# Kernel tuning notes

Hardware: AMD Instinct MI355X
Metric: run time of the kernel (lower is better)

The kernel has to match this reference:

```python
import jax, jax.numpy as jnp
import numpy as np

S, N, IN = 4096, 32, 4
H, IF, SF, OUT = 64, 8, 4, 2
N_PAIRS = N * (N - 1)


def setup_inputs() -> dict:
    key = jax.random.key(0)
    ks = jax.random.split(key, 12)
    f = jax.random.normal
    return {
        "inputs": f(ks[0], (S, N, IN), jnp.float32),
        "L1W": f(ks[1], (H, IN), jnp.float32) * 0.1,
        "L1b": f(ks[2], (H,), jnp.float32) * 0.1,
        "L2W": f(ks[3], (H, H), jnp.float32) * 0.1,
        "L2b": f(ks[4], (H,), jnp.float32) * 0.1,
        "I1W": f(ks[5], (H, H), jnp.float32) * 0.1,
        "I2W": f(ks[6], (IF, H), jnp.float32) * 0.1,
        "I3": f(ks[7], (N_PAIRS, OUT, IF // OUT), jnp.float32) * 0.01,
        "S1W": f(ks[8], (SF, IN), jnp.float32) * 0.1,
        "S1b": f(ks[9], (SF,), jnp.float32) * 0.1,
        "S2W": f(ks[10], (N, OUT, SF // OUT), jnp.float32) * 0.01,
        "S2b": jnp.zeros((N, OUT), jnp.float32),
    }


def reference(inputs, L1W, L1b, L2W, L2b, I1W, I2W, I3, S1W, S1b, S2W, S2b):
    seq_len, n_obj = inputs.shape[:2]
    out_size = S2b.shape[1]

    # shared encoders (torch Linear: x @ W.T + b)
    h = jax.nn.relu(inputs @ L1W.T + L1b)
    h = jax.nn.relu(h @ L2W.T + L2b)          # [S, N, H]
    hs = jax.nn.relu(inputs @ S1W.T + S1b)    # [S, N, SF]

    # all pairwise differences Xi - Xj -> edge MLP (no biases)
    diff = h[:, :, None, :] - h[:, None, :, :]      # [S, N, N, H]
    pair = jnp.tanh(diff @ I1W.T)                   # [S, N, N, H]
    pair = jnp.tanh(pair @ I2W.T)                   # [S, N, N, IF]
    k_int = pair.shape[-1] // out_size
    pair = pair.reshape(seq_len, n_obj, n_obj, out_size, k_int)

    # scatter per-pair weights I3 into dense [N, N, OUT, k] using the
    # row-major Table ordering (i, j != i); diagonal stays zero, which
    # matches the original since diag pairwise features are exactly 0.
    ii, jj = np.nonzero(~np.eye(n_obj, dtype=bool))
    I3d = jnp.zeros((n_obj, n_obj, out_size, k_int), I3.dtype).at[ii, jj].set(I3)

    interaction = jnp.einsum('sijdk,ijdk->sid', pair, I3d)  # [S, N, OUT]

    k_self = hs.shape[-1] // out_size
    hs = hs.reshape(seq_len, n_obj, out_size, k_self)
    self_term = jnp.einsum('sidk,idk->sid', hs, S2W) + S2b  # [S, N, OUT]

    return interaction + self_term
```

## Files before the change

### kernel.cpp

```cpp
#include <hip/hip_runtime.h>
#include <math.h>

#define SEQ   4096
#define NOBJ  32
#define IN_F  4
#define HID   64
#define IFEAT 8
#define NPAIR_HALF 496
#define NTILE 31

#define TWO_LOG2E 2.8853900817779268f
#define GP_CLAMP  10.0f

#if __has_builtin(__builtin_amdgcn_exp2f)
  #define EXP2F(x) __builtin_amdgcn_exp2f(x)
#else
  #define EXP2F(x) exp2f(x)
#endif

typedef _Float16 h2    __attribute__((ext_vector_type(2)));
typedef _Float16 f16x8 __attribute__((ext_vector_type(8)));
typedef short    s16x8 __attribute__((ext_vector_type(8)));
typedef float    f32x4 __attribute__((ext_vector_type(4)));

__device__ __forceinline__ h2 pack2(float a, float b) {
  return __builtin_bit_cast(h2, __builtin_amdgcn_cvt_pkrtz(a, b));
}
__device__ __forceinline__ unsigned pbits(h2 v) { return __builtin_bit_cast(unsigned, v); }

__device__ __forceinline__ f16x8 pack8(float4 a, float4 b) {
  int4 v;
  v.x = (int)pbits(pack2(a.x, a.y));
  v.y = (int)pbits(pack2(a.z, a.w));
  v.z = (int)pbits(pack2(b.x, b.y));
  v.w = (int)pbits(pack2(b.z, b.w));
  return __builtin_bit_cast(f16x8, v);
}

__device__ __forceinline__ f16x8 rcp8nr(f16x8 x) {
  const s16x8 magic = (short)0x7799;
  f16x8 r = __builtin_bit_cast(f16x8, (s16x8)(magic - __builtin_bit_cast(s16x8, x)));
  const f16x8 two = (_Float16)2.0f;
  const f16x8 nx = -x;
#if __has_builtin(__builtin_elementwise_fma)
  r = r * __builtin_elementwise_fma(nx, r, two);
  r = r * __builtin_elementwise_fma(nx, r, two);
#else
  r = r * (nx * r + two);
  r = r * (nx * r + two);
#endif
  return r;
}

__device__ __forceinline__ float dot2h(h2 a, h2 b, float c) {
#if __has_builtin(__builtin_amdgcn_fdot2)
  return __builtin_amdgcn_fdot2(a, b, c, false);
#else
  float r = c;
  r = fmaf((float)a.x, (float)b.x, r);
  r = fmaf((float)a.y, (float)b.y, r);
  return r;
#endif
}

__device__ __forceinline__ float xor8_f32(float v) {
#if __has_builtin(__builtin_amdgcn_mov_dpp)
  return __builtin_bit_cast(float,
      __builtin_amdgcn_mov_dpp(__builtin_bit_cast(int, v), 0x128, 0xF, 0xF, true));
#else
  return __shfl_xor(v, 8, 16);
#endif
}

__device__ __forceinline__ int pair_cum(int i) { return (i * (63 - i)) >> 1; }

__device__ __forceinline__ void pair_decode(int q, int& i, int& j) {
  int ii = (int)((63.0f - sqrtf(3969.0f - 8.0f * (float)q)) * 0.5f);
  if (ii > 0 && pair_cum(ii) > q) --ii;
  if (pair_cum(ii + 1) <= q)     ++ii;
  i = ii;
  j = ii + 1 + (q - pair_cum(ii));
}

__global__ __launch_bounds__(256, 4) void magnet_fused(
    const float* __restrict__ x,
    const float* __restrict__ L1W,
    const float* __restrict__ L1b,
    const float* __restrict__ L2W,
    const float* __restrict__ L2b,
    const float* __restrict__ I1W,
    const float* __restrict__ I2W,
    const float* __restrict__ I3,
    const float* __restrict__ S1W,
    const float* __restrict__ S1b,
    const float* __restrict__ S2W,
    const float* __restrict__ S2b,
    float* __restrict__ out)
{
  __shared__ __align__(16) float smem[8536];
  unsigned*       sEd0 = (unsigned*)(smem + 4960);
  unsigned*       wB   = (unsigned*)(smem + 7264);
  float*          part = smem + 7264;
  float*          sW   = smem + 8032;
  unsigned*       ptab32 = (unsigned*)(smem + 8040);
  float*          swpart = smem + 4960;

  const int t  = threadIdx.x;
  const int s0 = blockIdx.x * 2;

  if (t < 64) {
    const int f = t >> 3, seg = t & 7;
    const float4 a = *(const float4*)(I2W + f * HID + seg * 8);
    const float4 b = *(const float4*)(I2W + f * HID + seg * 8 + 4);
    swpart[t] = ((a.x + a.y) + (a.z + a.w)) + ((b.x + b.y) + (b.z + b.w));
  }
  #pragma unroll
  for (int idx = t; idx < 512; idx += 256) {
    const int n = idx >> 5, k2 = idx & 31;
    wB[idx] = (n < IFEAT)
      ? pbits(pack2(I2W[n * HID + 2 * k2], I2W[n * HID + 2 * k2 + 1])) : 0u;
  }
  #pragma unroll
  for (int q = t; q < NPAIR_HALF; q += 256) {
    int i, j; pair_decode(q, i, j);
    ptab32[q] = ((unsigned)(i * 36) << 16) | (unsigned)(j * 36);
  }

  {
    const int n = t & 31, gI = t >> 5, kb = gI * 8;
    const float4 xv0 = *(const float4*)(x + s0 * 128 + n * 4);
    const float4 xv1 = *(const float4*)(x + s0 * 128 + 128 + n * 4);
    float a[2][8];
    #pragma unroll
    for (int r = 0; r < 8; ++r) {
      const int k = kb + r;
      const float4 w = *(const float4*)(L1W + k * 4);
      const float bias = L1b[k];
      float v0 = bias, v1 = bias;
      v0 = fmaf(xv0.x, w.x, v0); v0 = fmaf(xv0.y, w.y, v0);
      v0 = fmaf(xv0.z, w.z, v0); v0 = fmaf(xv0.w, w.w, v0);
      v1 = fmaf(xv1.x, w.x, v1); v1 = fmaf(xv1.y, w.y, v1);
      v1 = fmaf(xv1.z, w.z, v1); v1 = fmaf(xv1.w, w.w, v1);
      a[0][r] = fmaxf(v0, 0.0f);
      a[1][r] = fmaxf(v1, 0.0f);
    }
    #pragma unroll
    for (int ss = 0; ss < 2; ++ss) {
      unsigned* sAtp = (unsigned*)(smem + ss * 1152);
      int4 pk;
      pk.x = (int)pbits(pack2(a[ss][0], a[ss][1]));
      pk.y = (int)pbits(pack2(a[ss][2], a[ss][3]));
      pk.z = (int)pbits(pack2(a[ss][4], a[ss][5]));
      pk.w = (int)pbits(pack2(a[ss][6], a[ss][7]));
      *(int4*)(sAtp + n * 36 + gI * 4) = pk;
    }
  }
  __syncthreads();

  if (t < IFEAT) {
    float a = 0.0f;
    #pragma unroll
    for (int c = 0; c < 8; ++c) a += swpart[t * 8 + c];
    sW[t] = a;
  }

  const int lane = t & 63;
  const int wv   = t >> 6;
  const int qd   = lane >> 4;
  const int ln   = lane & 15;

  {
    const int m = 16 * wv + ln;
    const float* wr = L2W + m * HID;
    const f16x8 A0 = pack8(*(const float4*)(wr + 8 * qd),
                           *(const float4*)(wr + 8 * qd + 4));
    const f16x8 A1 = pack8(*(const float4*)(wr + 32 + 8 * qd),
                           *(const float4*)(wr + 32 + 8 * qd + 4));
    const float4 bias = *(const float4*)(L2b + 16 * wv + 4 * qd);
    #pragma unroll
    for (int ss = 0; ss < 2; ++ss) {
      const unsigned* sAtp = (const unsigned*)(smem + ss * 1152);
      unsigned* sBtp = (unsigned*)(smem + 2480 + ss * 1152);
      #pragma unroll
      for (int nt = 0; nt < 2; ++nt) {
        const int n = nt * 16 + ln;
        const f16x8 B0 = __builtin_bit_cast(f16x8, *(const int4*)(sAtp + n * 36 + 4 * qd));
        const f16x8 B1 = __builtin_bit_cast(f16x8, *(const int4*)(sAtp + n * 36 + 16 + 4 * qd));
        f32x4 c; c[0] = bias.x; c[1] = bias.y; c[2] = bias.z; c[3] = bias.w;
        c = __builtin_amdgcn_mfma_f32_16x16x32_f16(A0, B0, c, 0, 0, 0);
        c = __builtin_amdgcn_mfma_f32_16x16x32_f16(A1, B1, c, 0, 0, 0);
        sBtp[n * 36 + 8 * wv + 2 * qd]     = pbits(pack2(fmaxf(c[0], 0.f), fmaxf(c[1], 0.f)));
        sBtp[n * 36 + 8 * wv + 2 * qd + 1] = pbits(pack2(fmaxf(c[2], 0.f), fmaxf(c[3], 0.f)));
      }
    }
  }
  __syncthreads();

  {
    const int m = 16 * wv + ln;
    const float* wr = I1W + m * HID;
    float4 w0 = *(const float4*)(wr + 8 * qd);
    float4 w1 = *(const float4*)(wr + 8 * qd + 4);
    float4 w2 = *(const float4*)(wr + 32 + 8 * qd);
    float4 w3 = *(const float4*)(wr + 32 + 8 * qd + 4);
    const float T = TWO_LOG2E;
    w0.x *= T; w0.y *= T; w0.z *= T; w0.w *= T;
    w1.x *= T; w1.y *= T; w1.z *= T; w1.w *= T;
    w2.x *= T; w2.y *= T; w2.z *= T; w2.w *= T;
    w3.x *= T; w3.y *= T; w3.z *= T; w3.w *= T;
    const f16x8 A0 = pack8(w0, w1);
    const f16x8 A1 = pack8(w2, w3);
    #pragma unroll
    for (int ss = 0; ss < 2; ++ss) {
      const unsigned* sBtp = (const unsigned*)(smem + 2480 + ss * 1152);
      unsigned* sEd = sEd0 + ss * 1152;
      #pragma unroll
      for (int nt = 0; nt < 2; ++nt) {
        const int n = nt * 16 + ln;
        const f16x8 B0 = __builtin_bit_cast(f16x8, *(const int4*)(sBtp + n * 36 + 4 * qd));
        const f16x8 B1 = __builtin_bit_cast(f16x8, *(const int4*)(sBtp + n * 36 + 16 + 4 * qd));
        f32x4 c; c[0] = 0.f; c[1] = 0.f; c[2] = 0.f; c[3] = 0.f;
        c = __builtin_amdgcn_mfma_f32_16x16x32_f16(A0, B0, c, 0, 0, 0);
        c = __builtin_amdgcn_mfma_f32_16x16x32_f16(A1, B1, c, 0, 0, 0);
        float e[4];
        #pragma unroll
        for (int r = 0; r < 4; ++r) {
          float gp = fminf(fmaxf(c[r], -GP_CLAMP), GP_CLAMP);
          e[r] = EXP2F(gp);
        }
        sEd[n * 36 + 8 * wv + 2 * qd]     = pbits(pack2(e[0], e[1]));
        sEd[n * 36 + 8 * wv + 2 * qd + 1] = pbits(pack2(e[2], e[3]));
      }
    }
  }
  __syncthreads();

  {
    const f16x8 B0 = __builtin_bit_cast(f16x8, *(const int4*)(wB + ln * 32 + 4 * qd));
    const f16x8 B1 = __builtin_bit_cast(f16x8, *(const int4*)(wB + ln * 32 + 16 + 4 * qd));
    const float WfT = sW[ln & 7] * TWO_LOG2E;
    const float n2T = -2.0f * TWO_LOG2E;
    const bool lo = (ln < IFEAT);
    _Float16* svb = lo ? (_Float16*)smem : (_Float16*)(smem + 2480);
    const int col = ln & 7;

    unsigned pijr[8];
    #pragma unroll
    for (int it = 0; it < 8; ++it) {
      const int tl = wv + it * 4;
      pijr[it] = ptab32[(tl < NTILE ? tl : 0) * 16 + ln];
    }

    #pragma unroll 2
    for (int it = 0; it < 8; ++it) {
      const int tile = wv + it * 4;
      if (tile < NTILE) {
        const unsigned pij = pijr[it];
        const int io = (int)(pij >> 16), jo = (int)(pij & 0xffffu);
        f32x4 c0, c1;
        #pragma unroll
        for (int ss = 0; ss < 2; ++ss) {
          const unsigned* sEd = sEd0 + ss * 1152;
          const f16x8 ei0 = __builtin_bit_cast(f16x8, *(const int4*)(sEd + io + 4 * qd));
          const f16x8 ei1 = __builtin_bit_cast(f16x8, *(const int4*)(sEd + io + 16 + 4 * qd));
          const f16x8 fj0 = __builtin_bit_cast(f16x8, *(const int4*)(sEd + jo + 4 * qd));
          const f16x8 fj1 = __builtin_bit_cast(f16x8, *(const int4*)(sEd + jo + 16 + 4 * qd));
          const f16x8 su0 = ei0 + fj0;
          const f16x8 su1 = ei1 + fj1;
          const f16x8 A0 = fj0 * rcp8nr(su0);
          const f16x8 A1 = fj1 * rcp8nr(su1);
          f32x4 c; c[0] = 0.f; c[1] = 0.f; c[2] = 0.f; c[3] = 0.f;
          c = __builtin_amdgcn_mfma_f32_16x16x32_f16(A0, B0, c, 0, 0, 0);
          c = __builtin_amdgcn_mfma_f32_16x16x32_f16(A1, B1, c, 0, 0, 0);
          if (ss == 0) c0 = c; else c1 = c;
        }
        #pragma unroll
        for (int r = 0; r < 4; ++r) {
          const float c1s = xor8_f32(c1[r]);
          const float m = lo ? c0[r] : c1s;
          const float arg = fmaf(n2T, m, WfT);
          const float e = EXP2F(arg);
          const float rr = __builtin_amdgcn_rcpf(e + 1.0f);
          const float v = fmaf(-2.0f, rr, 1.0f);
          svb[(tile * 16 + 4 * qd + r) * 10 + col] = (_Float16)v;
        }
      }
    }
  }
  __syncthreads();

  {
    const int ss = t >> 7, i = (t >> 2) & 31, d = (t >> 1) & 1, half = t & 1;
    const _Float16* sv = ss ? (const _Float16*)(smem + 2480) : (const _Float16*)smem;
    const int msta = half * 16;
    const int Ci = pair_cum(i);
    float sum = 0.0f;
    #pragma unroll
    for (int it = 0; it < 16; ++it) {
      const int m = msta + it;
      if (m < 31) {
        const bool up = (m >= i);
        const int q = up ? (Ci + m - i) : (pair_cum(m) + i - m - 1);
        const h2* vp = (const h2*)(sv + q * 10 + d * 4);
        const h2 va = vp[0], vb = vp[1];
        const float4 cf = *(const float4*)(I3 + (i * 31 + m) * 8 + d * 4);
        const h2 ca = pack2(cf.x, cf.y);
        const h2 cb = pack2(cf.z, cf.w);
        float dot = dot2h(va, ca, 0.0f);
        dot = dot2h(vb, cb, dot);
        const float sgn = up ? 1.0f : -1.0f;
        sum = fmaf(sgn, dot, sum);
      }
    }
    part[t] = sum;
  }
  __syncthreads();

  if (t < 128) {
    const int ss = t >> 6, i = (t >> 1) & 31, d = t & 1;
    const int pbase = ss * 128 + i * 4 + d * 2;
    float sum = part[pbase] + part[pbase + 1];

    float res = S2b[i * 2 + d] + sum;
    const float4 xv = *(const float4*)(x + (s0 + ss) * 128 + i * 4);
    #pragma unroll
    for (int k = 0; k < 2; ++k) {
      const int f = d * 2 + k;
      float hs = S1b[f];
      hs = fmaf(xv.x, S1W[f * 4 + 0], hs);
      hs = fmaf(xv.y, S1W[f * 4 + 1], hs);
      hs = fmaf(xv.z, S1W[f * 4 + 2], hs);
      hs = fmaf(xv.w, S1W[f * 4 + 3], hs);
      hs = fmaxf(hs, 0.0f);
      res = fmaf(hs, S2W[i * 4 + d * 2 + k], res);
    }
    out[(s0 + ss) * (NOBJ * 2) + i * 2 + d] = res;
  }
}

extern "C" void kernel_launch(void* const* d_in, const int* in_sizes, int n_in,
                              void* d_out, int out_size, void* d_ws, size_t ws_size,
                              hipStream_t stream) {
  const float* x   = (const float*)d_in[0];
  const float* L1W = (const float*)d_in[1];
  const float* L1b = (const float*)d_in[2];
  const float* L2W = (const float*)d_in[3];
  const float* L2b = (const float*)d_in[4];
  const float* I1W = (const float*)d_in[5];
  const float* I2W = (const float*)d_in[6];
  const float* I3  = (const float*)d_in[7];
  const float* S1W = (const float*)d_in[8];
  const float* S1b = (const float*)d_in[9];
  const float* S2W = (const float*)d_in[10];
  const float* S2b = (const float*)d_in[11];
  float* outp = (float*)d_out;

  magnet_fused<<<SEQ / 2, 256, 0, stream>>>(x, L1W, L1b, L2W, L2b, I1W, I2W, I3,
                                            S1W, S1b, S2W, S2b, outp);
}
```

Before: 108.9 us.

## Split the two sequences across wave groups using 512-thread blocks

Blocks grow from 256 to 512 threads, and each group of four waves now handles one of the block's two sequence steps instead of looping over both. This covers the L1/L2/I1 encoders, the pairwise MFMA stage and the final I3 reduction, which now uses four partial sums per output instead of two. In the pair stage, the low and high lanes split the MFMA output rows between them through the xor-8 exchange, so the old cross-sequence select is no longer needed. The goal is to shorten each thread's serial work and raise the number of waves in flight. The cost is higher register pressure under launch_bounds(512,4), and synchronisation barriers now span twice as many waves.

```diff
diff --git a/kernel.cpp b/kernel.cpp
--- a/kernel.cpp
+++ b/kernel.cpp
@@ -82,7 +82,7 @@
   j = ii + 1 + (q - pair_cum(ii));
 }
 
-__global__ __launch_bounds__(256, 4) void magnet_fused(
+__global__ __launch_bounds__(512, 4) void magnet_fused(
     const float* __restrict__ x,
     const float* __restrict__ L1W,
     const float* __restrict__ L1b,
@@ -114,46 +114,36 @@
     const float4 b = *(const float4*)(I2W + f * HID + seg * 8 + 4);
     swpart[t] = ((a.x + a.y) + (a.z + a.w)) + ((b.x + b.y) + (b.z + b.w));
   }
-  #pragma unroll
-  for (int idx = t; idx < 512; idx += 256) {
-    const int n = idx >> 5, k2 = idx & 31;
-    wB[idx] = (n < IFEAT)
+  {
+    const int n = t >> 5, k2 = t & 31;
+    wB[t] = (n < IFEAT)
       ? pbits(pack2(I2W[n * HID + 2 * k2], I2W[n * HID + 2 * k2 + 1])) : 0u;
   }
-  #pragma unroll
-  for (int q = t; q < NPAIR_HALF; q += 256) {
-    int i, j; pair_decode(q, i, j);
-    ptab32[q] = ((unsigned)(i * 36) << 16) | (unsigned)(j * 36);
-  }
-
-  {
-    const int n = t & 31, gI = t >> 5, kb = gI * 8;
-    const float4 xv0 = *(const float4*)(x + s0 * 128 + n * 4);
-    const float4 xv1 = *(const float4*)(x + s0 * 128 + 128 + n * 4);
-    float a[2][8];
+  if (t < NPAIR_HALF) {
+    int i, j; pair_decode(t, i, j);
+    ptab32[t] = ((unsigned)(i * 36) << 16) | (unsigned)(j * 36);
+  }
+
+  {
+    const int n = t & 31, gI = (t >> 5) & 7, ssp = t >> 8, kb = gI * 8;
+    const float4 xv = *(const float4*)(x + s0 * 128 + ssp * 128 + n * 4);
+    float a[8];
     #pragma unroll
     for (int r = 0; r < 8; ++r) {
       const int k = kb + r;
       const float4 w = *(const float4*)(L1W + k * 4);
-      const float bias = L1b[k];
-      float v0 = bias, v1 = bias;
-      v0 = fmaf(xv0.x, w.x, v0); v0 = fmaf(xv0.y, w.y, v0);
-      v0 = fmaf(xv0.z, w.z, v0); v0 = fmaf(xv0.w, w.w, v0);
-      v1 = fmaf(xv1.x, w.x, v1); v1 = fmaf(xv1.y, w.y, v1);
-      v1 = fmaf(xv1.z, w.z, v1); v1 = fmaf(xv1.w, w.w, v1);
-      a[0][r] = fmaxf(v0, 0.0f);
-      a[1][r] = fmaxf(v1, 0.0f);
-    }
-    #pragma unroll
-    for (int ss = 0; ss < 2; ++ss) {
-      unsigned* sAtp = (unsigned*)(smem + ss * 1152);
-      int4 pk;
-      pk.x = (int)pbits(pack2(a[ss][0], a[ss][1]));
-      pk.y = (int)pbits(pack2(a[ss][2], a[ss][3]));
-      pk.z = (int)pbits(pack2(a[ss][4], a[ss][5]));
-      pk.w = (int)pbits(pack2(a[ss][6], a[ss][7]));
-      *(int4*)(sAtp + n * 36 + gI * 4) = pk;
-    }
+      float v = L1b[k];
+      v = fmaf(xv.x, w.x, v); v = fmaf(xv.y, w.y, v);
+      v = fmaf(xv.z, w.z, v); v = fmaf(xv.w, w.w, v);
+      a[r] = fmaxf(v, 0.0f);
+    }
+    unsigned* sAtp = (unsigned*)(smem + ssp * 1152);
+    int4 pk;
+    pk.x = (int)pbits(pack2(a[0], a[1]));
+    pk.y = (int)pbits(pack2(a[2], a[3]));
+    pk.z = (int)pbits(pack2(a[4], a[5]));
+    pk.w = (int)pbits(pack2(a[6], a[7]));
+    *(int4*)(sAtp + n * 36 + gI * 4) = pk;
   }
   __syncthreads();
 
@@ -166,38 +156,37 @@
 
   const int lane = t & 63;
   const int wv   = t >> 6;
+  const int wq   = wv & 3;
+  const int ssw  = wv >> 2;
   const int qd   = lane >> 4;
   const int ln   = lane & 15;
 
   {
-    const int m = 16 * wv + ln;
+    const int m = 16 * wq + ln;
     const float* wr = L2W + m * HID;
     const f16x8 A0 = pack8(*(const float4*)(wr + 8 * qd),
                            *(const float4*)(wr + 8 * qd + 4));
     const f16x8 A1 = pack8(*(const float4*)(wr + 32 + 8 * qd),
                            *(const float4*)(wr + 32 + 8 * qd + 4));
-    const float4 bias = *(const float4*)(L2b + 16 * wv + 4 * qd);
-    #pragma unroll
-    for (int ss = 0; ss < 2; ++ss) {
-      const unsigned* sAtp = (const unsigned*)(smem + ss * 1152);
-      unsigned* sBtp = (unsigned*)(smem + 2480 + ss * 1152);
-      #pragma unroll
-      for (int nt = 0; nt < 2; ++nt) {
-        const int n = nt * 16 + ln;
-        const f16x8 B0 = __builtin_bit_cast(f16x8, *(const int4*)(sAtp + n * 36 + 4 * qd));
-        const f16x8 B1 = __builtin_bit_cast(f16x8, *(const int4*)(sAtp + n * 36 + 16 + 4 * qd));
-        f32x4 c; c[0] = bias.x; c[1] = bias.y; c[2] = bias.z; c[3] = bias.w;
-        c = __builtin_amdgcn_mfma_f32_16x16x32_f16(A0, B0, c, 0, 0, 0);
-        c = __builtin_amdgcn_mfma_f32_16x16x32_f16(A1, B1, c, 0, 0, 0);
-        sBtp[n * 36 + 8 * wv + 2 * qd]     = pbits(pack2(fmaxf(c[0], 0.f), fmaxf(c[1], 0.f)));
-        sBtp[n * 36 + 8 * wv + 2 * qd + 1] = pbits(pack2(fmaxf(c[2], 0.f), fmaxf(c[3], 0.f)));
-      }
-    }
-  }
-  __syncthreads();
-
-  {
-    const int m = 16 * wv + ln;
+    const float4 bias = *(const float4*)(L2b + 16 * wq + 4 * qd);
+    const unsigned* sAtp = (const unsigned*)(smem + ssw * 1152);
+    unsigned* sBtp = (unsigned*)(smem + 2480 + ssw * 1152);
+    #pragma unroll
+    for (int nt = 0; nt < 2; ++nt) {
+      const int n = nt * 16 + ln;
+      const f16x8 B0 = __builtin_bit_cast(f16x8, *(const int4*)(sAtp + n * 36 + 4 * qd));
+      const f16x8 B1 = __builtin_bit_cast(f16x8, *(const int4*)(sAtp + n * 36 + 16 + 4 * qd));
+      f32x4 c; c[0] = bias.x; c[1] = bias.y; c[2] = bias.z; c[3] = bias.w;
+      c = __builtin_amdgcn_mfma_f32_16x16x32_f16(A0, B0, c, 0, 0, 0);
+      c = __builtin_amdgcn_mfma_f32_16x16x32_f16(A1, B1, c, 0, 0, 0);
+      sBtp[n * 36 + 8 * wq + 2 * qd]     = pbits(pack2(fmaxf(c[0], 0.f), fmaxf(c[1], 0.f)));
+      sBtp[n * 36 + 8 * wq + 2 * qd + 1] = pbits(pack2(fmaxf(c[2], 0.f), fmaxf(c[3], 0.f)));
+    }
+  }
+  __syncthreads();
+
+  {
+    const int m = 16 * wq + ln;
     const float* wr = I1W + m * HID;
     float4 w0 = *(const float4*)(wr + 8 * qd);
     float4 w1 = *(const float4*)(wr + 8 * qd + 4);
@@ -210,27 +199,24 @@
     w3.x *= T; w3.y *= T; w3.z *= T; w3.w *= T;
     const f16x8 A0 = pack8(w0, w1);
     const f16x8 A1 = pack8(w2, w3);
-    #pragma unroll
-    for (int ss = 0; ss < 2; ++ss) {
-      const unsigned* sBtp = (const unsigned*)(smem + 2480 + ss * 1152);
-      unsigned* sEd = sEd0 + ss * 1152;
+    const unsigned* sBtp = (const unsigned*)(smem + 2480 + ssw * 1152);
+    unsigned* sEd = sEd0 + ssw * 1152;
+    #pragma unroll
+    for (int nt = 0; nt < 2; ++nt) {
+      const int n = nt * 16 + ln;
+      const f16x8 B0 = __builtin_bit_cast(f16x8, *(const int4*)(sBtp + n * 36 + 4 * qd));
+      const f16x8 B1 = __builtin_bit_cast(f16x8, *(const int4*)(sBtp + n * 36 + 16 + 4 * qd));
+      f32x4 c; c[0] = 0.f; c[1] = 0.f; c[2] = 0.f; c[3] = 0.f;
+      c = __builtin_amdgcn_mfma_f32_16x16x32_f16(A0, B0, c, 0, 0, 0);
+      c = __builtin_amdgcn_mfma_f32_16x16x32_f16(A1, B1, c, 0, 0, 0);
+      float e[4];
       #pragma unroll
-      for (int nt = 0; nt < 2; ++nt) {
-        const int n = nt * 16 + ln;
-        const f16x8 B0 = __builtin_bit_cast(f16x8, *(const int4*)(sBtp + n * 36 + 4 * qd));
-        const f16x8 B1 = __builtin_bit_cast(f16x8, *(const int4*)(sBtp + n * 36 + 16 + 4 * qd));
-        f32x4 c; c[0] = 0.f; c[1] = 0.f; c[2] = 0.f; c[3] = 0.f;
-        c = __builtin_amdgcn_mfma_f32_16x16x32_f16(A0, B0, c, 0, 0, 0);
-        c = __builtin_amdgcn_mfma_f32_16x16x32_f16(A1, B1, c, 0, 0, 0);
-        float e[4];
-        #pragma unroll
-        for (int r = 0; r < 4; ++r) {
-          float gp = fminf(fmaxf(c[r], -GP_CLAMP), GP_CLAMP);
-          e[r] = EXP2F(gp);
-        }
-        sEd[n * 36 + 8 * wv + 2 * qd]     = pbits(pack2(e[0], e[1]));
-        sEd[n * 36 + 8 * wv + 2 * qd + 1] = pbits(pack2(e[2], e[3]));
+      for (int r = 0; r < 4; ++r) {
+        float gp = fminf(fmaxf(c[r], -GP_CLAMP), GP_CLAMP);
+        e[r] = EXP2F(gp);
       }
+      sEd[n * 36 + 8 * wq + 2 * qd]     = pbits(pack2(e[0], e[1]));
+      sEd[n * 36 + 8 * wq + 2 * qd + 1] = pbits(pack2(e[2], e[3]));
     }
   }
   __syncthreads();
@@ -241,48 +227,44 @@
     const float WfT = sW[ln & 7] * TWO_LOG2E;
     const float n2T = -2.0f * TWO_LOG2E;
     const bool lo = (ln < IFEAT);
-    _Float16* svb = lo ? (_Float16*)smem : (_Float16*)(smem + 2480);
+    const unsigned* sEd = sEd0 + ssw * 1152;
+    _Float16* svb = ssw ? (_Float16*)(smem + 2480) : (_Float16*)smem;
     const int col = ln & 7;
+    const int rofs = lo ? 0 : 1;
 
     unsigned pijr[8];
     #pragma unroll
     for (int it = 0; it < 8; ++it) {
-      const int tl = wv + it * 4;
+      const int tl = wq + it * 4;
       pijr[it] = ptab32[(tl < NTILE ? tl : 0) * 16 + ln];
     }
 
     #pragma unroll 2
     for (int it = 0; it < 8; ++it) {
-      const int tile = wv + it * 4;
+      const int tile = wq + it * 4;
       if (tile < NTILE) {
         const unsigned pij = pijr[it];
         const int io = (int)(pij >> 16), jo = (int)(pij & 0xffffu);
-        f32x4 c0, c1;
+        const f16x8 ei0 = __builtin_bit_cast(f16x8, *(const int4*)(sEd + io + 4 * qd));
+        const f16x8 ei1 = __builtin_bit_cast(f16x8, *(const int4*)(sEd + io + 16 + 4 * qd));
+        const f16x8 fj0 = __builtin_bit_cast(f16x8, *(const int4*)(sEd + jo + 4 * qd));
+        const f16x8 fj1 = __builtin_bit_cast(f16x8, *(const int4*)(sEd + jo + 16 + 4 * qd));
+        const f16x8 su0 = ei0 + fj0;
+        const f16x8 su1 = ei1 + fj1;
+        const f16x8 A0 = fj0 * rcp8nr(su0);
+        const f16x8 A1 = fj1 * rcp8nr(su1);
+        f32x4 c; c[0] = 0.f; c[1] = 0.f; c[2] = 0.f; c[3] = 0.f;
+        c = __builtin_amdgcn_mfma_f32_16x16x32_f16(A0, B0, c, 0, 0, 0);
+        c = __builtin_amdgcn_mfma_f32_16x16x32_f16(A1, B1, c, 0, 0, 0);
         #pragma unroll
-        for (int ss = 0; ss < 2; ++ss) {
-          const unsigned* sEd = sEd0 + ss * 1152;
-          const f16x8 ei0 = __builtin_bit_cast(f16x8, *(const int4*)(sEd + io + 4 * qd));
-          const f16x8 ei1 = __builtin_bit_cast(f16x8, *(const int4*)(sEd + io + 16 + 4 * qd));
-          const f16x8 fj0 = __builtin_bit_cast(f16x8, *(const int4*)(sEd + jo + 4 * qd));
-          const f16x8 fj1 = __builtin_bit_cast(f16x8, *(const int4*)(sEd + jo + 16 + 4 * qd));
-          const f16x8 su0 = ei0 + fj0;
-          const f16x8 su1 = ei1 + fj1;
-          const f16x8 A0 = fj0 * rcp8nr(su0);
-          const f16x8 A1 = fj1 * rcp8nr(su1);
-          f32x4 c; c[0] = 0.f; c[1] = 0.f; c[2] = 0.f; c[3] = 0.f;
-          c = __builtin_amdgcn_mfma_f32_16x16x32_f16(A0, B0, c, 0, 0, 0);
-          c = __builtin_amdgcn_mfma_f32_16x16x32_f16(A1, B1, c, 0, 0, 0);
-          if (ss == 0) c0 = c; else c1 = c;
-        }
-        #pragma unroll
-        for (int r = 0; r < 4; ++r) {
-          const float c1s = xor8_f32(c1[r]);
-          const float m = lo ? c0[r] : c1s;
+        for (int rb = 0; rb < 4; rb += 2) {
+          const float cns = xor8_f32(c[rb + 1]);
+          const float m = lo ? c[rb] : cns;
           const float arg = fmaf(n2T, m, WfT);
           const float e = EXP2F(arg);
           const float rr = __builtin_amdgcn_rcpf(e + 1.0f);
           const float v = fmaf(-2.0f, rr, 1.0f);
-          svb[(tile * 16 + 4 * qd + r) * 10 + col] = (_Float16)v;
+          svb[(tile * 16 + 4 * qd + rb + rofs) * 10 + col] = (_Float16)v;
         }
       }
     }
@@ -290,13 +272,13 @@
   __syncthreads();
 
   {
-    const int ss = t >> 7, i = (t >> 2) & 31, d = (t >> 1) & 1, half = t & 1;
-    const _Float16* sv = ss ? (const _Float16*)(smem + 2480) : (const _Float16*)smem;
-    const int msta = half * 16;
+    const int ssp = t >> 8, i = (t >> 3) & 31, d = (t >> 2) & 1, mq = t & 3;
+    const _Float16* sv = ssp ? (const _Float16*)(smem + 2480) : (const _Float16*)smem;
+    const int msta = mq * 8;
     const int Ci = pair_cum(i);
     float sum = 0.0f;
     #pragma unroll
-    for (int it = 0; it < 16; ++it) {
+    for (int it = 0; it < 8; ++it) {
       const int m = msta + it;
       if (m < 31) {
         const bool up = (m >= i);
@@ -317,12 +299,12 @@
   __syncthreads();
 
   if (t < 128) {
-    const int ss = t >> 6, i = (t >> 1) & 31, d = t & 1;
-    const int pbase = ss * 128 + i * 4 + d * 2;
-    float sum = part[pbase] + part[pbase + 1];
+    const int ssp = t >> 6, i = (t >> 1) & 31, d = t & 1;
+    const int pbase = ssp * 256 + i * 8 + d * 4;
+    float sum = (part[pbase] + part[pbase + 1]) + (part[pbase + 2] + part[pbase + 3]);
 
     float res = S2b[i * 2 + d] + sum;
-    const float4 xv = *(const float4*)(x + (s0 + ss) * 128 + i * 4);
+    const float4 xv = *(const float4*)(x + (s0 + ssp) * 128 + i * 4);
     #pragma unroll
     for (int k = 0; k < 2; ++k) {
       const int f = d * 2 + k;
@@ -334,7 +316,7 @@
       hs = fmaxf(hs, 0.0f);
       res = fmaf(hs, S2W[i * 4 + d * 2 + k], res);
     }
-    out[(s0 + ss) * (NOBJ * 2) + i * 2 + d] = res;
+    out[(s0 + ssp) * (NOBJ * 2) + i * 2 + d] = res;
   }
 }
 
@@ -355,6 +337,6 @@
   const float* S2b = (const float*)d_in[11];
   float* outp = (float*)d_out;
 
-  magnet_fused<<<SEQ / 2, 256, 0, stream>>>(x, L1W, L1b, L2W, L2b, I1W, I2W, I3,
+  magnet_fused<<<SEQ / 2, 512, 0, stream>>>(x, L1W, L1b, L2W, L2b, I1W, I2W, I3,
                                             S1W, S1b, S2W, S2b, outp);
 }
```

After: 116.3 us. 1.07x slower.

## Process four sequence steps per block and drop the partial-sum reduction stage

Applied to the files above, without the earlier changes.

Each block now handles four sequence positions instead of two, which halves the grid and reuses the per-block weight setup (I2W packing, pair table, L2W/I1W fragments) across more work. Shared memory grows to about 62KB, which may reduce blocks per CU below the launch_bounds target. The final interaction reduction now has one thread per (s,i,d) loop over all 31 partners, removing a separate partial-sum pass and one barrier at the cost of longer serial loops. The pair-tile loop also drops the register-prefetched pair table in favour of direct loads.

```diff
diff --git a/kernel.cpp b/kernel.cpp
--- a/kernel.cpp
+++ b/kernel.cpp
@@ -97,16 +97,15 @@
     const float* __restrict__ S2b,
     float* __restrict__ out)
 {
-  __shared__ __align__(16) float smem[8536];
-  unsigned*       sEd0 = (unsigned*)(smem + 4960);
-  unsigned*       wB   = (unsigned*)(smem + 7264);
-  float*          part = smem + 7264;
-  float*          sW   = smem + 8032;
-  unsigned*       ptab32 = (unsigned*)(smem + 8040);
-  float*          swpart = smem + 4960;
+  __shared__ __align__(16) float smem[15544];
+  unsigned*       sEd0 = (unsigned*)(smem + 9920);
+  unsigned*       wB   = (unsigned*)(smem + 14528);
+  float*          sW   = smem + 15040;
+  unsigned*       ptab32 = (unsigned*)(smem + 15048);
+  float*          swpart = smem + 9920;
 
   const int t  = threadIdx.x;
-  const int s0 = blockIdx.x * 2;
+  const int s0 = blockIdx.x * 4;
 
   if (t < 64) {
     const int f = t >> 3, seg = t & 7;
@@ -128,24 +127,26 @@
 
   {
     const int n = t & 31, gI = t >> 5, kb = gI * 8;
-    const float4 xv0 = *(const float4*)(x + s0 * 128 + n * 4);
-    const float4 xv1 = *(const float4*)(x + s0 * 128 + 128 + n * 4);
-    float a[2][8];
+    float4 xv[4];
+    #pragma unroll
+    for (int ss = 0; ss < 4; ++ss)
+      xv[ss] = *(const float4*)(x + (s0 + ss) * 128 + n * 4);
+    float a[4][8];
     #pragma unroll
     for (int r = 0; r < 8; ++r) {
       const int k = kb + r;
       const float4 w = *(const float4*)(L1W + k * 4);
       const float bias = L1b[k];
-      float v0 = bias, v1 = bias;
-      v0 = fmaf(xv0.x, w.x, v0); v0 = fmaf(xv0.y, w.y, v0);
-      v0 = fmaf(xv0.z, w.z, v0); v0 = fmaf(xv0.w, w.w, v0);
-      v1 = fmaf(xv1.x, w.x, v1); v1 = fmaf(xv1.y, w.y, v1);
-      v1 = fmaf(xv1.z, w.z, v1); v1 = fmaf(xv1.w, w.w, v1);
-      a[0][r] = fmaxf(v0, 0.0f);
-      a[1][r] = fmaxf(v1, 0.0f);
-    }
-    #pragma unroll
-    for (int ss = 0; ss < 2; ++ss) {
+      #pragma unroll
+      for (int ss = 0; ss < 4; ++ss) {
+        float v = bias;
+        v = fmaf(xv[ss].x, w.x, v); v = fmaf(xv[ss].y, w.y, v);
+        v = fmaf(xv[ss].z, w.z, v); v = fmaf(xv[ss].w, w.w, v);
+        a[ss][r] = fmaxf(v, 0.0f);
+      }
+    }
+    #pragma unroll
+    for (int ss = 0; ss < 4; ++ss) {
       unsigned* sAtp = (unsigned*)(smem + ss * 1152);
       int4 pk;
       pk.x = (int)pbits(pack2(a[ss][0], a[ss][1]));
@@ -178,9 +179,9 @@
                            *(const float4*)(wr + 32 + 8 * qd + 4));
     const float4 bias = *(const float4*)(L2b + 16 * wv + 4 * qd);
     #pragma unroll
-    for (int ss = 0; ss < 2; ++ss) {
+    for (int ss = 0; ss < 4; ++ss) {
       const unsigned* sAtp = (const unsigned*)(smem + ss * 1152);
-      unsigned* sBtp = (unsigned*)(smem + 2480 + ss * 1152);
+      unsigned* sBtp = (unsigned*)(smem + 4608 + ss * 1152);
       #pragma unroll
       for (int nt = 0; nt < 2; ++nt) {
         const int n = nt * 16 + ln;
@@ -211,8 +212,8 @@
     const f16x8 A0 = pack8(w0, w1);
     const f16x8 A1 = pack8(w2, w3);
     #pragma unroll
-    for (int ss = 0; ss < 2; ++ss) {
-      const unsigned* sBtp = (const unsigned*)(smem + 2480 + ss * 1152);
+    for (int ss = 0; ss < 4; ++ss) {
+      const unsigned* sBtp = (const unsigned*)(smem + 4608 + ss * 1152);
       unsigned* sEd = sEd0 + ss * 1152;
       #pragma unroll
       for (int nt = 0; nt < 2; ++nt) {
@@ -241,26 +242,17 @@
     const float WfT = sW[ln & 7] * TWO_LOG2E;
     const float n2T = -2.0f * TWO_LOG2E;
     const bool lo = (ln < IFEAT);
-    _Float16* svb = lo ? (_Float16*)smem : (_Float16*)(smem + 2480);
     const int col = ln & 7;
 
-    unsigned pijr[8];
-    #pragma unroll
-    for (int it = 0; it < 8; ++it) {
-      const int tl = wv + it * 4;
-      pijr[it] = ptab32[(tl < NTILE ? tl : 0) * 16 + ln];
-    }
-
-    #pragma unroll 2
-    for (int it = 0; it < 8; ++it) {
-      const int tile = wv + it * 4;
-      if (tile < NTILE) {
-        const unsigned pij = pijr[it];
-        const int io = (int)(pij >> 16), jo = (int)(pij & 0xffffu);
+    for (int tile = wv; tile < NTILE; tile += 4) {
+      const unsigned pij = ptab32[tile * 16 + ln];
+      const int io = (int)(pij >> 16), jo = (int)(pij & 0xffffu);
+      #pragma unroll
+      for (int sp = 0; sp < 2; ++sp) {
         f32x4 c0, c1;
         #pragma unroll
-        for (int ss = 0; ss < 2; ++ss) {
-          const unsigned* sEd = sEd0 + ss * 1152;
+        for (int half = 0; half < 2; ++half) {
+          const unsigned* sEd = sEd0 + (2 * sp + half) * 1152;
           const f16x8 ei0 = __builtin_bit_cast(f16x8, *(const int4*)(sEd + io + 4 * qd));
           const f16x8 ei1 = __builtin_bit_cast(f16x8, *(const int4*)(sEd + io + 16 + 4 * qd));
           const f16x8 fj0 = __builtin_bit_cast(f16x8, *(const int4*)(sEd + jo + 4 * qd));
@@ -272,8 +264,10 @@
           f32x4 c; c[0] = 0.f; c[1] = 0.f; c[2] = 0.f; c[3] = 0.f;
           c = __builtin_amdgcn_mfma_f32_16x16x32_f16(A0, B0, c, 0, 0, 0);
           c = __builtin_amdgcn_mfma_f32_16x16x32_f16(A1, B1, c, 0, 0, 0);
-          if (ss == 0) c0 = c; else c1 = c;
+          if (half == 0) c0 = c; else c1 = c;
         }
+        _Float16* svb = lo ? ((_Float16*)smem + (2 * sp) * 4960)
+                           : ((_Float16*)smem + (2 * sp + 1) * 4960);
         #pragma unroll
         for (int r = 0; r < 4; ++r) {
           const float c1s = xor8_f32(c1[r]);
@@ -290,36 +284,24 @@
   __syncthreads();
 
   {
-    const int ss = t >> 7, i = (t >> 2) & 31, d = (t >> 1) & 1, half = t & 1;
-    const _Float16* sv = ss ? (const _Float16*)(smem + 2480) : (const _Float16*)smem;
-    const int msta = half * 16;
+    const int ss = t >> 6, i = (t >> 1) & 31, d = t & 1;
+    const _Float16* sv = (const _Float16*)smem + ss * 4960;
     const int Ci = pair_cum(i);
     float sum = 0.0f;
     #pragma unroll
-    for (int it = 0; it < 16; ++it) {
-      const int m = msta + it;
-      if (m < 31) {
-        const bool up = (m >= i);
-        const int q = up ? (Ci + m - i) : (pair_cum(m) + i - m - 1);
-        const h2* vp = (const h2*)(sv + q * 10 + d * 4);
-        const h2 va = vp[0], vb = vp[1];
-        const float4 cf = *(const float4*)(I3 + (i * 31 + m) * 8 + d * 4);
-        const h2 ca = pack2(cf.x, cf.y);
-        const h2 cb = pack2(cf.z, cf.w);
-        float dot = dot2h(va, ca, 0.0f);
-        dot = dot2h(vb, cb, dot);
-        const float sgn = up ? 1.0f : -1.0f;
-        sum = fmaf(sgn, dot, sum);
-      }
-    }
-    part[t] = sum;
-  }
-  __syncthreads();
-
-  if (t < 128) {
-    const int ss = t >> 6, i = (t >> 1) & 31, d = t & 1;
-    const int pbase = ss * 128 + i * 4 + d * 2;
-    float sum = part[pbase] + part[pbase + 1];
+    for (int m = 0; m < 31; ++m) {
+      const bool up = (m >= i);
+      const int q = up ? (Ci + m - i) : (pair_cum(m) + i - m - 1);
+      const h2* vp = (const h2*)(sv + q * 10 + d * 4);
+      const h2 va = vp[0], vb = vp[1];
+      const float4 cf = *(const float4*)(I3 + (i * 31 + m) * 8 + d * 4);
+      const h2 ca = pack2(cf.x, cf.y);
+      const h2 cb = pack2(cf.z, cf.w);
+      float dot = dot2h(va, ca, 0.0f);
+      dot = dot2h(vb, cb, dot);
+      const float sgn = up ? 1.0f : -1.0f;
+      sum = fmaf(sgn, dot, sum);
+    }
 
     float res = S2b[i * 2 + d] + sum;
     const float4 xv = *(const float4*)(x + (s0 + ss) * 128 + i * 4);
@@ -355,6 +337,6 @@
   const float* S2b = (const float*)d_in[11];
   float* outp = (float*)d_out;
 
-  magnet_fused<<<SEQ / 2, 256, 0, stream>>>(x, L1W, L1b, L2W, L2b, I1W, I2W, I3,
+  magnet_fused<<<SEQ / 4, 256, 0, stream>>>(x, L1W, L1b, L2W, L2b, I1W, I2W, I3,
                                             S1W, S1b, S2W, S2b, outp);
 }
```

After: 109.6 us. Within noise of the previous version (+0.6%).
